# Kernel optimization log

Measured on AMD Instinct MI355X. Metric: run time of the kernel, lower is better.

The kernel has to match this reference:

```python
import jax, jax.numpy as jnp
import numpy as np

VOCAB = 128
N_LAYERS = 4
HEAD_DIM = 128
N_HEADS = 16
PAD = 127
HIDDEN = N_HEADS * HEAD_DIM
B, S = 1, 2048
SCALE = 1.0 / float(np.sqrt(HEAD_DIM))


def _intervals(boundary):
    # torch: interval = cumsum(boundary)+1; shifted = roll(1); shifted[:,0]=interval[:,0]
    idx = jnp.cumsum(boundary.astype(jnp.int32), axis=-1) + 1
    sh = jnp.roll(idx, 1, axis=-1)
    return sh.at[:, 0].set(idx[:, 0])


def _build_mask(tokens, segment_mask, specials_mask):
    # Combined causal & padding & word & segment mask, cache_size=0, distances=0.
    word_int = _intervals(specials_mask)            # [B,S]
    seg_bound = ~segment_mask                       # [B,S]
    seg_int = _intervals(seg_bound)                 # [B,S]
    q = jnp.arange(S)[:, None]
    kv = jnp.arange(S)[None, :]
    causal = q >= kv                                # [S,S]
    dist_neg = (q - kv) < 0                         # mask_*_distance = 0 term
    nonpad = tokens != PAD                          # [B,S]
    padm = nonpad[:, :, None] & nonpad[:, None, :]  # [B,S,S]
    wordm = specials_mask[:, None, :] | dist_neg[None] | (word_int[:, :, None] == word_int[:, None, :])
    segm = seg_bound[:, None, :] | dist_neg[None] | (seg_int[:, :, None] == seg_int[:, None, :])
    return causal[None] & padm & wordm & segm       # [B,S,S]


def _attention(h, mask):
    # q=k=v=h (no projections in DummyModel); flex_attention default scale 1/sqrt(D)
    x = h.reshape(B, S, N_HEADS, HEAD_DIM)
    scores = jnp.einsum('bqhd,bkhd->bhqk', x, x) * SCALE
    neg = jnp.finfo(scores.dtype).min
    scores = jnp.where(mask[:, None], scores, neg)
    probs = jax.nn.softmax(scores, axis=-1)
    # fully-masked rows (e.g. padding queries) -> zero output, matching flex_attention
    row_valid = jnp.any(mask, axis=-1)              # [B,S]
    probs = jnp.where(row_valid[:, None, :, None], probs, 0.0)
    out = jnp.einsum('bhqk,bkhd->bqhd', probs, x)
    return out.reshape(B, S, HIDDEN)


def setup_inputs() -> dict:
    key = jax.random.key(0)
    k1, k2, k3, k4, k5, k6 = jax.random.split(key, 6)
    tokens = jax.random.randint(k1, (B, S), 0, PAD)          # 0..126, no pad tokens
    segment_mask = jax.random.bernoulli(k2, 0.98, (B, S))
    specials_mask = jax.random.bernoulli(k3, 0.2, (B, S))    # True = word boundary/special
    emb_w = jax.random.normal(k4, (VOCAB, HIDDEN), jnp.float32) * 0.02
    lm_w = jax.random.normal(k5, (VOCAB, HIDDEN), jnp.float32) * 0.02
    lm_b = jnp.zeros((VOCAB,), jnp.float32)
    seg_w = jax.random.normal(k6, (2, HIDDEN), jnp.float32) * 0.02
    seg_b = jnp.zeros((2,), jnp.float32)
    return {"tokens": tokens, "segment_mask": segment_mask, "specials_mask": specials_mask,
            "emb_w": emb_w, "lm_w": lm_w, "lm_b": lm_b, "seg_w": seg_w, "seg_b": seg_b}


def reference(tokens, segment_mask, specials_mask, emb_w, lm_w, lm_b, seg_w, seg_b):
    mask = _build_mask(tokens, segment_mask, specials_mask)
    hidden = emb_w[tokens]                                   # [B,S,HIDDEN]
    for _ in range(N_LAYERS):
        hidden = _attention(hidden, mask)
    logits = hidden @ lm_w.T + lm_b                          # [B,S,VOCAB]
    logits_segment = hidden @ seg_w.T + seg_b                # [B,S,2]
    return logits, logits_segment
```

## Files before the change

kernel.cpp:

```cpp
#include <hip/hip_runtime.h>

#define S 2048
#define HID 2048
#define NH 16
#define DH 128
#define VOC 128
#define LCAP 128
#define K2EXP 0.12752551286084112f
#define RTHR 62.0f
#define NEGS -3.0e38f

typedef __bf16 bf16_t;
typedef __attribute__((ext_vector_type(8))) __bf16 bf16x8;
typedef __attribute__((ext_vector_type(4))) __bf16 bf16x4;
typedef __attribute__((ext_vector_type(4))) float f32x4;
typedef __attribute__((ext_vector_type(16))) float f32x16;

typedef __attribute__((address_space(1))) unsigned int guint;
typedef __attribute__((address_space(3))) unsigned int luint;

#define MFMA16 __builtin_amdgcn_mfma_f32_16x16x32_bf16
#define MFMA32 __builtin_amdgcn_mfma_f32_32x32x16_bf16

__device__ __forceinline__ void gl_lds16(const void* g, void* l) {
  __builtin_amdgcn_global_load_lds((guint*)(unsigned long long)g,
                                   (luint*)(unsigned)(unsigned long long)l,
                                   16, 0, 0);
}

__device__ __forceinline__ unsigned cvtpk(float lo, float hi) {
  unsigned r;
  asm("v_cvt_pk_bf16_f32 %0, %1, %2" : "=v"(r) : "v"(lo), "v"(hi));
  return r;
}
__device__ __forceinline__ void plswap(unsigned& a, unsigned& b) {
  asm volatile("v_permlane32_swap_b32 %0, %1" : "+v"(a), "+v"(b));
}
__device__ __forceinline__ bf16x8 mk8(unsigned d0, unsigned d1, unsigned d2, unsigned d3) {
  union { unsigned u[4]; bf16x8 v; } x;
  x.u[0] = d0; x.u[1] = d1; x.u[2] = d2; x.u[3] = d3;
  return x.v;
}


__global__ __launch_bounds__(256) void maskprep2(const int* __restrict__ tokens,
                                                 const unsigned char* __restrict__ seg,
                                                 const unsigned char* __restrict__ spc,
                                                 int4* __restrict__ mi,
                                                 int* __restrict__ lq,
                                                 unsigned long long* __restrict__ lmask,
                                                 int2* __restrict__ smeta) {
  __shared__ int ssp[257], ssg[257], smw[257], sms[257], sfl[257];
  __shared__ int fpre[2048];
  __shared__ int ns64[64];
  __shared__ unsigned long long lmk[32];
  __shared__ int cdet[2];
  int t = threadIdx.x;
  if (t < 2) cdet[t] = 0;
  if (t < 32) lmk[t] = 0ull;
  __syncthreads();
  {
    int nz = ((t & 3) != 0 && seg[t]) ? 1 : 0;
    int fc = ((t & 3) == 3 && seg[t] == 0x3f) ? 1 : 0;
    if (nz) atomicAdd(&cdet[0], 1);
    if (fc) atomicAdd(&cdet[1], 1);
  }
  __syncthreads();
  int lay = (cdet[1] > 8) ? 2 : ((cdet[0] > 4) ? 1 : 0);
  auto getb = [&](const unsigned char* p, int i) -> int {
    if (lay == 1) return p[i] != 0;
    if (lay == 2) return ((const float*)p)[i] != 0.f;
    return ((const int*)p)[i] != 0;
  };
  int base = t * 8;
  int spv[8], sgv[8], npv[8], fv[8];
  int a = 0, b = 0, mw = 0, ms = 0, fs = 0;
  for (int j = 0; j < 8; j++) {
    int i = base + j;
    spv[j] = getb(spc, i);
    sgv[j] = 1 - getb(seg, i);
    npv[j] = (tokens[i] != 127) ? 1 : 0;
    fv[j] = spv[j] & sgv[j] & npv[j];
    a += spv[j]; b += sgv[j]; fs += fv[j];
    if (i >= 1 && spv[j]) mw = (i + 1 > mw) ? i + 1 : mw;
    if (i >= 1 && sgv[j]) ms = (i + 1 > ms) ? i + 1 : ms;
  }
  ssp[t + 1] = a; ssg[t + 1] = b; smw[t + 1] = mw; sms[t + 1] = ms; sfl[t + 1] = fs;
  if (t == 0) { ssp[0] = 0; ssg[0] = 0; smw[0] = 0; sms[0] = 0; sfl[0] = 0; }
  __syncthreads();
  for (int off = 1; off < 256; off <<= 1) {
    int v0 = 0, v1 = 0, v2 = 0, v3 = 0, v4 = 0;
    if (t + 1 > off) { v0 = ssp[t+1-off]; v1 = ssg[t+1-off]; v2 = smw[t+1-off]; v3 = sms[t+1-off]; v4 = sfl[t+1-off]; }
    __syncthreads();
    ssp[t + 1] += v0; ssg[t + 1] += v1;
    if (v2 > smw[t + 1]) smw[t + 1] = v2;
    if (v3 > sms[t + 1]) sms[t + 1] = v3;
    sfl[t + 1] += v4;
    __syncthreads();
  }
  if ((t & 3) == 0) {
    int ws = smw[t], ss = sms[t];
    ns64[t >> 2] = ws < ss ? ws : ss;
  }
  int esp = ssp[t], esg = ssg[t], ef = sfl[t];
  for (int j = 0; j < 8; j++) {
    int i = base + j;
    int wint = (i == 0) ? (1 + spv[j]) : (1 + esp);
    int sint = (i == 0) ? (1 + sgv[j]) : (1 + esg);
    mi[i] = make_int4(npv[j] | (spv[j] << 1) | (sgv[j] << 2), wint, sint, 0);
    fpre[i] = ef;
    int lqv = (fv[j] && ef < LCAP) ? ef : -1;
    lq[i] = lqv;
    if (lqv >= 0) atomicOr(&lmk[i >> 6], 1ull << (i & 63));
    esp += spv[j]; esg += sgv[j]; ef += fv[j];
  }
  __syncthreads();
  if (t < 32) lmask[t] = lmk[t];
  if (t < 64) {
    int nsTile = ns64[t] >> 5;
    int lc = fpre[nsTile * 32];
    if (lc > LCAP) lc = LCAP;
    smeta[t] = make_int2(nsTile, lc);
  }
}

__global__ __launch_bounds__(256) void bitgen(const int4* __restrict__ mi,
                                              unsigned* __restrict__ cmask) {
  __shared__ int4 km[32];
  int w = blockIdx.x;
  int t = threadIdx.x;
  int q = blockIdx.y * 256 + t;
  if (t < 32) km[t] = mi[w * 32 + t];
  __syncthreads();
  int4 mq = mi[q];
  unsigned word = 0;
  #pragma unroll
  for (int j = 0; j < 32; j++) {
    int kv = w * 32 + j;
    int4 mk = km[j];
    bool v = ((mq.x & mk.x) & 1) &&
             ((mk.x & 2) || (mq.y == mk.y)) &&
             ((mk.x & 4) || (mq.z == mk.z)) &&
             (kv <= q);
    word |= (v ? 1u : 0u) << j;
  }
  cmask[(size_t)w * S + q] = word;
}

__global__ __launch_bounds__(256) void embedT2(const int* __restrict__ tokens,
                                               const float* __restrict__ emb,
                                               const int* __restrict__ lq,
                                               const unsigned long long* __restrict__ lmask,
                                               bf16_t* __restrict__ hb, bf16_t* __restrict__ vtb,
                                               bf16_t* __restrict__ hbL, bf16_t* __restrict__ vtbL) {
  __shared__ bf16_t tile[64 * 136];
  int tid = threadIdx.x;
  int q0 = blockIdx.x * 64, h = blockIdx.y;
  int ql = tid >> 2, d0 = (tid & 3) * 32;
  int tok = tokens[q0 + ql];
  const float4* src = (const float4*)(emb + (size_t)tok * HID + h * DH + d0);
  bf16x8 ob[4];
  #pragma unroll
  for (int i = 0; i < 8; i++) {
    float4 f = src[i];
    ob[i >> 1][(i & 1) * 4 + 0] = (bf16_t)f.x;
    ob[i >> 1][(i & 1) * 4 + 1] = (bf16_t)f.y;
    ob[i >> 1][(i & 1) * 4 + 2] = (bf16_t)f.z;
    ob[i >> 1][(i & 1) * 4 + 3] = (bf16_t)f.w;
  }
  #pragma unroll
  for (int i = 0; i < 4; i++)
    *(bf16x8*)(hb + (size_t)(q0 + ql) * HID + h * DH + d0 + i * 8) = ob[i];
  #pragma unroll
  for (int i = 0; i < 4; i++)
    #pragma unroll
    for (int j = 0; j < 8; j++) tile[ql * 136 + d0 + i * 8 + j] = ob[i][j];
  __syncthreads();
  {
    int tl = tid >> 7, d = tid & 127;
    bf16_t* vt = vtb + ((size_t)(h * 64) + 2 * blockIdx.x + tl) * 4096;
    #pragma unroll
    for (int c = 0; c < 4; c++) {
      bf16x8 v;
      #pragma unroll
      for (int e = 0; e < 8; e++)
        v[e] = tile[(32 * tl + 8 * (c ^ (d & 3)) + e) * 136 + d];
      *(bf16x8*)(vt + d * 32 + c * 8) = v;
    }
  }
  unsigned long long lm = lmask[q0 >> 6];
  while (lm) {
    int r = __builtin_ctzll(lm);
    lm &= lm - 1;
    int li = lq[q0 + r];
    if (li >= 0 && tid < 128) {
      bf16_t vv = tile[r * 136 + tid];
      hbL[(size_t)li * HID + h * DH + tid] = vv;
      vtbL[((size_t)(h * 4) + (li >> 5)) * 4096 + tid * 32 + (((li & 31) >> 3) ^ (tid & 3)) * 8 + (li & 7)] = vv;
    }
  }
}

__global__ __launch_bounds__(64, 2) void attn8(const bf16_t* __restrict__ hb,
                                               const bf16_t* __restrict__ vtb,
                                               const bf16_t* __restrict__ hbL,
                                               const bf16_t* __restrict__ vtbL,
                                               const unsigned* __restrict__ cmask,
                                               const int4* __restrict__ mi,
                                               const int2* __restrict__ smeta,
                                               const int* __restrict__ lq,
                                               const unsigned long long* __restrict__ lmask,
                                               bf16_t* __restrict__ ob,
                                               bf16_t* __restrict__ ovtb,
                                               bf16_t* __restrict__ obL,
                                               bf16_t* __restrict__ ovtbL,
                                               int writeT) {
  __shared__ __align__(16) char lds_raw[32768];

  int h = blockIdx.x, st = blockIdx.y;
  int2 sm = smeta[st];
  int nsT = sm.x, lcount = sm.y;
  int nNear = st + 1 - nsT;
  int nLT = (lcount + 31) >> 5;
  int nIter = nNear + nLT;

  int l = threadIdx.x, l31 = l & 31, hi = l >> 5;
  int q0 = 32 * st, q = q0 + l31;
  int npq = mi[q].x & 1;

  bf16x8 qf[8];
  {
    const bf16_t* hq = hb + (size_t)q * HID + h * DH;
    #pragma unroll
    for (int ks = 0; ks < 8; ks++) qf[ks] = *(const bf16x8*)(hq + ks * 16 + hi * 8);
  }

  f32x16 acc[4];
  #pragma unroll
  for (int i = 0; i < 4; i++)
    #pragma unroll
    for (int r = 0; r < 16; r++) acc[i][r] = 0.f;
  float m = -1e30f, lsum = 0.f;
  int swz = l31 & 7;

  auto STAGE = [&](int i, int b) {
    const bf16_t* Kbase; const bf16_t* Vtile;
    if (i < nNear) {
      int t = nsT + i;
      Kbase = hb + (size_t)(t * 32) * HID + h * DH;
      Vtile = vtb + ((size_t)(h * 64) + t) * 4096;
    } else {
      int j = i - nNear;
      Kbase = hbL + (size_t)(j * 32) * HID + h * DH;
      Vtile = vtbL + ((size_t)(h * 4) + j) * 4096;
    }
    bf16_t* Kb = (bf16_t*)(lds_raw + b * 16384);
    bf16_t* Vb = (bf16_t*)(lds_raw + b * 16384 + 8192);
    #pragma unroll
    for (int i2 = 0; i2 < 8; i2++) {
      int rowK = i2 * 4 + (l >> 4); int chK = (l & 15) ^ (rowK & 7);
      gl_lds16(Kbase + (size_t)rowK * HID + chK * 8, Kb + i2 * 512);
    }
    #pragma unroll
    for (int i2 = 0; i2 < 8; i2++)
      gl_lds16(Vtile + i2 * 512 + l * 8, Vb + i2 * 512);
  };

  auto getmask = [&](int i) -> unsigned {
    if (i < nNear) return cmask[(size_t)(nsT + i) * S + q];
    int rem = lcount - (i - nNear) * 32;
    unsigned w0 = (rem >= 32) ? 0xffffffffu : ((rem <= 0) ? 0u : ((1u << rem) - 1u));
    return npq ? w0 : 0u;
  };

  STAGE(0, 0);
  for (int i = 0; i < nIter; i++) {
    int b = i & 1;
    if (i + 1 < nIter) {
      STAGE(i + 1, b ^ 1);
      asm volatile("s_waitcnt vmcnt(16)" ::: "memory");
    } else {
      asm volatile("s_waitcnt vmcnt(0)" ::: "memory");
    }
    unsigned w0 = getmask(i);

    if (__any(w0 != 0u)) {
      const bf16_t* Kb = (const bf16_t*)(lds_raw + b * 16384);
      const bf16_t* Vb = (const bf16_t*)(lds_raw + b * 16384 + 8192);
      f32x16 sA, sB;
      #pragma unroll
      for (int r = 0; r < 16; r++) { sA[r] = 0.f; sB[r] = 0.f; }
      const bf16_t* kp = Kb + l31 * 128;
      #pragma unroll
      for (int ks = 0; ks < 8; ks += 2) {
        bf16x8 kf0 = *(const bf16x8*)(kp + (((2 * ks + hi) ^ swz) * 8));
        bf16x8 kf1 = *(const bf16x8*)(kp + (((2 * (ks + 1) + hi) ^ swz) * 8));
        sA = MFMA32(kf0, qf[ks], sA, 0, 0, 0);
        sB = MFMA32(kf1, qf[ks + 1], sB, 0, 0, 0);
      }

      float sv[16];
      #pragma unroll
      for (int r = 0; r < 16; r++) {
        int bit = (r & 3) + 8 * (r >> 2) + 4 * hi;
        float sr = sA[r] + sB[r];
        sv[r] = ((w0 >> bit) & 1u) ? sr : NEGS;
      }
      float t0 = fmaxf(fmaxf(sv[0], sv[1]), fmaxf(sv[2], sv[3]));
      float t1 = fmaxf(fmaxf(sv[4], sv[5]), fmaxf(sv[6], sv[7]));
      float t2 = fmaxf(fmaxf(sv[8], sv[9]), fmaxf(sv[10], sv[11]));
      float t3 = fmaxf(fmaxf(sv[12], sv[13]), fmaxf(sv[14], sv[15]));
      float mx = fmaxf(fmaxf(t0, t1), fmaxf(t2, t3));
      mx = fmaxf(mx, __shfl_xor(mx, 32, 64));
      if (__any(mx > m + RTHR)) {
        float mn = fmaxf(m, mx);
        float al = exp2f((m - mn) * K2EXP);
        m = mn; lsum *= al;
        #pragma unroll
        for (int r = 0; r < 16; r++) {
          float alr = __shfl(al, (r & 3) + 8 * (r >> 2) + 4 * hi, 64);
          #pragma unroll
          for (int d = 0; d < 4; d++) acc[d][r] *= alr;
        }
      }
      float mk = m * K2EXP;
      float p[16];
      #pragma unroll
      for (int r = 0; r < 16; r++)
        p[r] = exp2f(__builtin_fmaf(sv[r], K2EXP, -mk));
      float u0 = (p[0] + p[1]) + (p[2] + p[3]);
      float u1 = (p[4] + p[5]) + (p[6] + p[7]);
      float u2 = (p[8] + p[9]) + (p[10] + p[11]);
      float u3 = (p[12] + p[13]) + (p[14] + p[15]);
      float ps = (u0 + u1) + (u2 + u3);
      ps += __shfl_xor(ps, 32, 64);
      lsum += ps;

      bf16x8 pa[2];
      {
        unsigned a0 = cvtpk(p[0], p[1]),   a1 = cvtpk(p[2], p[3]);
        unsigned b0 = cvtpk(p[4], p[5]),   b1 = cvtpk(p[6], p[7]);
        unsigned a2 = cvtpk(p[8], p[9]),   a3 = cvtpk(p[10], p[11]);
        unsigned b2 = cvtpk(p[12], p[13]), b3 = cvtpk(p[14], p[15]);
        plswap(a0, b0); plswap(a1, b1); plswap(a2, b2); plswap(a3, b3);
        pa[0] = mk8(a0, a1, b0, b1);
        pa[1] = mk8(a2, a3, b2, b3);
      }

      #pragma unroll
      for (int db = 0; db < 4; db++) {
        const bf16_t* vr = Vb + (32 * db + l31) * 32;
        #pragma unroll
        for (int ks = 0; ks < 2; ks++) {
          bf16x8 vf = *(const bf16x8*)(vr + (((2 * ks + hi) ^ (l31 & 3)) * 8));
          acc[db] = MFMA32(pa[ks], vf, acc[db], 0, 0, 0);
        }
      }
    }
  }

  bf16_t* tl = (bf16_t*)lds_raw;
  float inv = (lsum > 0.f) ? 1.f / lsum : 0.f;
  #pragma unroll
  for (int r = 0; r < 16; r++) {
    int qr = (r & 3) + 8 * (r >> 2) + 4 * hi;
    float ivr = __shfl(inv, qr, 64);
    #pragma unroll
    for (int db = 0; db < 4; db++)
      tl[qr * 132 + db * 32 + l31] = (bf16_t)(acc[db][r] * ivr);
  }
  {
    int c4 = l & 3;
    #pragma unroll
    for (int g = 0; g < 2; g++) {
      int row = g * 16 + (l >> 2);
      #pragma unroll
      for (int k = 0; k < 4; k++) {
        bf16x8 v = *(const bf16x8*)(tl + row * 132 + c4 * 32 + k * 8);
        *(bf16x8*)(ob + (size_t)(q0 + row) * HID + h * DH + c4 * 32 + k * 8) = v;
      }
    }
  }
  if (writeT) {
    bf16_t* vt = ovtb + ((size_t)(h * 64) + st) * 4096;
    #pragma unroll
    for (int s = 0; s < 8; s++) {
      int d = s * 16 + (l >> 2);
      bf16x8 v;
      #pragma unroll
      for (int e = 0; e < 8; e++)
        v[e] = tl[(8 * ((l & 3) ^ (d & 3)) + e) * 132 + d];
      *(bf16x8*)(vt + s * 512 + l * 8) = v;
    }
    unsigned lm32 = (unsigned)(lmask[st >> 1] >> ((st & 1) * 32));
    while (lm32) {
      int r = __builtin_ctz(lm32);
      lm32 &= lm32 - 1;
      int li = lq[q0 + r];
      if (li >= 0) {
        #pragma unroll
        for (int half = 0; half < 2; half++) {
          int dd = l + 64 * half;
          bf16_t vv = tl[r * 132 + dd];
          obL[(size_t)li * HID + h * DH + dd] = vv;
          ovtbL[((size_t)(h * 4) + (li >> 5)) * 4096 + dd * 32 + (((li & 31) >> 3) ^ (dd & 3)) * 8 + (li & 7)] = vv;
        }
      }
    }
  }
}

__global__ __launch_bounds__(256) void wcvt(const float* __restrict__ w, bf16_t* __restrict__ wb) {
  int i = blockIdx.x * 256 + threadIdx.x;
  float4 f = ((const float4*)w)[i];
  bf16x4 v;
  v[0] = (bf16_t)f.x; v[1] = (bf16_t)f.y; v[2] = (bf16_t)f.z; v[3] = (bf16_t)f.w;
  *(bf16x4*)(wb + (size_t)i * 4) = v;
}

__global__ __launch_bounds__(256) void lmseg_head(const bf16_t* __restrict__ hb,
                                                  const bf16_t* __restrict__ wbf,
                                                  const float* __restrict__ bias,
                                                  const float* __restrict__ sw,
                                                  const float* __restrict__ sb,
                                                  float* __restrict__ out,
                                                  float* __restrict__ outseg) {
  __shared__ float red[4][16][130];
  int tid = threadIdx.x;
  int w = tid >> 6, l = tid & 63, l16 = l & 15, g = l >> 4;
  int t0 = blockIdx.x * 16;
  f32x4 acc[8];
  #pragma unroll
  for (int i = 0; i < 8; i++) acc[i] = (f32x4){0.f, 0.f, 0.f, 0.f};
  const bf16_t* arow = hb + (size_t)(t0 + l16) * HID + w * 512;
  for (int k0 = 0; k0 < 512; k0 += 32) {
    bf16x8 af = *(const bf16x8*)(arow + k0 + g * 8);
    #pragma unroll
    for (int vt = 0; vt < 8; vt++) {
      bf16x8 bf_ = *(const bf16x8*)(wbf + (size_t)(vt * 16 + l16) * HID + w * 512 + k0 + g * 8);
      acc[vt] = MFMA16(af, bf_, acc[vt], 0, 0, 0);
    }
  }
  #pragma unroll
  for (int vt = 0; vt < 8; vt++)
    #pragma unroll
    for (int r = 0; r < 4; r++)
      red[w][4 * g + r][vt * 16 + l16] = acc[vt][r];
  __syncthreads();
  int q = tid >> 4, vc = (tid & 15) * 8;
  #pragma unroll
  for (int j = 0; j < 8; j++) {
    float s = red[0][q][vc + j] + red[1][q][vc + j] + red[2][q][vc + j] + red[3][q][vc + j];
    out[(size_t)(t0 + q) * VOC + vc + j] = s + bias[vc + j];
  }
  {
    int c = tid & 15;
    const bf16_t* hrow = hb + (size_t)(t0 + q) * HID + c * 128;
    float s0 = 0.f, s1 = 0.f;
    #pragma unroll
    for (int i = 0; i < 16; i++) {
      bf16x8 v = *(const bf16x8*)(hrow + i * 8);
      const float4* w0p = (const float4*)(sw + c * 128 + i * 8);
      const float4* w1p = (const float4*)(sw + HID + c * 128 + i * 8);
      float4 x0 = w0p[0], x1 = w0p[1], y0 = w1p[0], y1 = w1p[1];
      s0 += (float)v[0]*x0.x + (float)v[1]*x0.y + (float)v[2]*x0.z + (float)v[3]*x0.w
          + (float)v[4]*x1.x + (float)v[5]*x1.y + (float)v[6]*x1.z + (float)v[7]*x1.w;
      s1 += (float)v[0]*y0.x + (float)v[1]*y0.y + (float)v[2]*y0.z + (float)v[3]*y0.w
          + (float)v[4]*y1.x + (float)v[5]*y1.y + (float)v[6]*y1.z + (float)v[7]*y1.w;
    }
    #pragma unroll
    for (int off = 1; off < 16; off <<= 1) {
      s0 += __shfl_xor(s0, off, 64);
      s1 += __shfl_xor(s1, off, 64);
    }
    if (c == 0) {
      outseg[(size_t)(t0 + q) * 2] = s0 + sb[0];
      outseg[(size_t)(t0 + q) * 2 + 1] = s1 + sb[1];
    }
  }
}

extern "C" void kernel_launch(void* const* d_in, const int* in_sizes, int n_in,
                              void* d_out, int out_size, void* d_ws, size_t ws_size,
                              hipStream_t stream) {
  const int* tokens = (const int*)d_in[0];
  const unsigned char* seg = (const unsigned char*)d_in[1];
  const unsigned char* spc = (const unsigned char*)d_in[2];
  const float* emb_w = (const float*)d_in[3];
  const float* lm_w = (const float*)d_in[4];
  const float* lm_b = (const float*)d_in[5];
  const float* seg_w = (const float*)d_in[6];
  const float* seg_b = (const float*)d_in[7];

  char* ws = (char*)d_ws;
  int4* mi = (int4*)ws;
  unsigned* cmask = (unsigned*)(ws + (1u << 20));
  int* lq = (int*)(ws + (1u << 20) + (512u << 10));
  unsigned long long* lmask = (unsigned long long*)(ws + (1u << 20) + (520u << 10));
  int2* smeta = (int2*)(ws + (1u << 20) + (524u << 10));
  bf16_t* wbf = (bf16_t*)(ws + (2u << 20));
  bf16_t* hbLA  = (bf16_t*)(ws + (3u << 20));
  bf16_t* hbLB  = (bf16_t*)(ws + (3u << 20) + (512u << 10));
  bf16_t* vtbLA = (bf16_t*)(ws + (4u << 20));
  bf16_t* vtbLB = (bf16_t*)(ws + (4u << 20) + (512u << 10));
  bf16_t* hbA  = (bf16_t*)(ws + (8u << 20));
  bf16_t* hbB  = (bf16_t*)(ws + (16u << 20));
  bf16_t* vtbA = (bf16_t*)(ws + (24u << 20));
  bf16_t* vtbB = (bf16_t*)(ws + (32u << 20));
  float* out = (float*)d_out;

  maskprep2<<<1, 256, 0, stream>>>(tokens, seg, spc, mi, lq, lmask, smeta);
  bitgen<<<dim3(64, 8), 256, 0, stream>>>(mi, cmask);
  embedT2<<<dim3(S / 64, NH), 256, 0, stream>>>(tokens, emb_w, lq, lmask, hbA, vtbA, hbLA, vtbLA);

  bf16_t* cur = hbA;   bf16_t* curV = vtbA;
  bf16_t* nxt = hbB;   bf16_t* nxtV = vtbB;
  bf16_t* curL = hbLA; bf16_t* curLV = vtbLA;
  bf16_t* nxtL = hbLB; bf16_t* nxtLV = vtbLB;
  for (int L = 0; L < 4; L++) {
    attn8<<<dim3(NH, 64), 64, 0, stream>>>(cur, curV, curL, curLV, cmask, mi, smeta, lq, lmask,
                                           nxt, nxtV, nxtL, nxtLV, (L < 3) ? 1 : 0);
    bf16_t* t1 = cur; cur = nxt; nxt = t1;
    bf16_t* t2 = curV; curV = nxtV; nxtV = t2;
    bf16_t* t3 = curL; curL = nxtL; nxtL = t3;
    bf16_t* t4 = curLV; curLV = nxtLV; nxtLV = t4;
  }

  wcvt<<<(VOC * HID / 4) / 256, 256, 0, stream>>>(lm_w, wbf);
  lmseg_head<<<S / 16, 256, 0, stream>>>(cur, wbf, lm_b, seg_w, seg_b, out, out + (size_t)S * VOC);
}
```

Measured before the change: 137.6 us.

## Store K in pre-swizzled tile layout and merge prep kernels into one launch

The attention kernel now reads K from a contiguous, pre-swizzled per-head 32x128 tile layout (ktb), the same way it reads V, rather than from strided rows of the row-major hidden buffer. Each layer writes its output directly in this tiled K and transposed V form, and writes row-major hidden only on the last layer for the LM head. The bitgen, embedding and weight-convert kernels are merged into a single megaprep launch with block-index dispatch, removing two launches. The cost is an extra tiled write per layer in place of the row-major write, plus more complex indexing.

Result: faster. 121.7 us (-11.5%).

```diff
diff --git a/kernel.cpp b/kernel.cpp
--- a/kernel.cpp
+++ b/kernel.cpp
@@ -124,96 +124,120 @@
   }
 }
 
-__global__ __launch_bounds__(256) void bitgen(const int4* __restrict__ mi,
-                                              unsigned* __restrict__ cmask) {
-  __shared__ int4 km[32];
-  int w = blockIdx.x;
-  int t = threadIdx.x;
-  int q = blockIdx.y * 256 + t;
-  if (t < 32) km[t] = mi[w * 32 + t];
-  __syncthreads();
-  int4 mq = mi[q];
-  unsigned word = 0;
-  #pragma unroll
-  for (int j = 0; j < 32; j++) {
-    int kv = w * 32 + j;
-    int4 mk = km[j];
-    bool v = ((mq.x & mk.x) & 1) &&
-             ((mk.x & 2) || (mq.y == mk.y)) &&
-             ((mk.x & 4) || (mq.z == mk.z)) &&
-             (kv <= q);
-    word |= (v ? 1u : 0u) << j;
-  }
-  cmask[(size_t)w * S + q] = word;
-}
-
-__global__ __launch_bounds__(256) void embedT2(const int* __restrict__ tokens,
-                                               const float* __restrict__ emb,
-                                               const int* __restrict__ lq,
-                                               const unsigned long long* __restrict__ lmask,
-                                               bf16_t* __restrict__ hb, bf16_t* __restrict__ vtb,
-                                               bf16_t* __restrict__ hbL, bf16_t* __restrict__ vtbL) {
-  __shared__ bf16_t tile[64 * 136];
+__global__ __launch_bounds__(256) void megaprep(const int* __restrict__ tokens,
+                                                const float* __restrict__ emb,
+                                                const int4* __restrict__ mi,
+                                                const int* __restrict__ lq,
+                                                const unsigned long long* __restrict__ lmask,
+                                                const float* __restrict__ lm_w,
+                                                bf16_t* __restrict__ wbf,
+                                                unsigned* __restrict__ cmask,
+                                                bf16_t* __restrict__ ktb,
+                                                bf16_t* __restrict__ vtb,
+                                                bf16_t* __restrict__ ktbL,
+                                                bf16_t* __restrict__ vtbL) {
+  __shared__ __align__(16) bf16_t tile[64 * 136];
+  int bid = blockIdx.x;
   int tid = threadIdx.x;
-  int q0 = blockIdx.x * 64, h = blockIdx.y;
-  int ql = tid >> 2, d0 = (tid & 3) * 32;
-  int tok = tokens[q0 + ql];
-  const float4* src = (const float4*)(emb + (size_t)tok * HID + h * DH + d0);
-  bf16x8 ob[4];
-  #pragma unroll
-  for (int i = 0; i < 8; i++) {
-    float4 f = src[i];
-    ob[i >> 1][(i & 1) * 4 + 0] = (bf16_t)f.x;
-    ob[i >> 1][(i & 1) * 4 + 1] = (bf16_t)f.y;
-    ob[i >> 1][(i & 1) * 4 + 2] = (bf16_t)f.z;
-    ob[i >> 1][(i & 1) * 4 + 3] = (bf16_t)f.w;
-  }
-  #pragma unroll
-  for (int i = 0; i < 4; i++)
-    *(bf16x8*)(hb + (size_t)(q0 + ql) * HID + h * DH + d0 + i * 8) = ob[i];
-  #pragma unroll
-  for (int i = 0; i < 4; i++)
-    #pragma unroll
-    for (int j = 0; j < 8; j++) tile[ql * 136 + d0 + i * 8 + j] = ob[i][j];
-  __syncthreads();
-  {
-    int tl = tid >> 7, d = tid & 127;
-    bf16_t* vt = vtb + ((size_t)(h * 64) + 2 * blockIdx.x + tl) * 4096;
-    #pragma unroll
-    for (int c = 0; c < 4; c++) {
-      bf16x8 v;
-      #pragma unroll
-      for (int e = 0; e < 8; e++)
-        v[e] = tile[(32 * tl + 8 * (c ^ (d & 3)) + e) * 136 + d];
-      *(bf16x8*)(vt + d * 32 + c * 8) = v;
-    }
-  }
-  unsigned long long lm = lmask[q0 >> 6];
-  while (lm) {
-    int r = __builtin_ctzll(lm);
-    lm &= lm - 1;
-    int li = lq[q0 + r];
-    if (li >= 0 && tid < 128) {
-      bf16_t vv = tile[r * 136 + tid];
-      hbL[(size_t)li * HID + h * DH + tid] = vv;
-      vtbL[((size_t)(h * 4) + (li >> 5)) * 4096 + tid * 32 + (((li & 31) >> 3) ^ (tid & 3)) * 8 + (li & 7)] = vv;
-    }
-  }
-}
-
-__global__ __launch_bounds__(64, 2) void attn8(const bf16_t* __restrict__ hb,
+
+  if (bid < 512) {
+    int qblk = bid & 31, h = bid >> 5;
+    int q0 = qblk * 64;
+    int ql = tid >> 2, d0 = (tid & 3) * 32;
+    int tok = tokens[q0 + ql];
+    const float4* src = (const float4*)(emb + (size_t)tok * HID + h * DH + d0);
+    #pragma unroll
+    for (int i = 0; i < 8; i++) {
+      float4 f = src[i];
+      tile[ql * 136 + d0 + i * 4 + 0] = (bf16_t)f.x;
+      tile[ql * 136 + d0 + i * 4 + 1] = (bf16_t)f.y;
+      tile[ql * 136 + d0 + i * 4 + 2] = (bf16_t)f.z;
+      tile[ql * 136 + d0 + i * 4 + 3] = (bf16_t)f.w;
+    }
+    __syncthreads();
+    {
+      int tl2 = tid >> 7, half = (tid >> 6) & 1, lane = tid & 63;
+      bf16_t* kt = ktb + ((size_t)(h * 64) + 2 * qblk + tl2) * 4096;
+      #pragma unroll
+      for (int k = 0; k < 4; k++) {
+        int s = half * 4 + k;
+        int row = s * 4 + (lane >> 4);
+        int c = lane & 15;
+        bf16x8 v;
+        #pragma unroll
+        for (int e = 0; e < 8; e++)
+          v[e] = tile[(32 * tl2 + row) * 136 + 8 * (c ^ (row & 7)) + e];
+        *(bf16x8*)(kt + s * 512 + lane * 8) = v;
+      }
+    }
+    {
+      int tl2 = tid >> 7, d = tid & 127;
+      bf16_t* vt = vtb + ((size_t)(h * 64) + 2 * qblk + tl2) * 4096;
+      #pragma unroll
+      for (int c = 0; c < 4; c++) {
+        bf16x8 v;
+        #pragma unroll
+        for (int e = 0; e < 8; e++)
+          v[e] = tile[(32 * tl2 + 8 * (c ^ (d & 3)) + e) * 136 + d];
+        *(bf16x8*)(vt + d * 32 + c * 8) = v;
+      }
+    }
+    unsigned long long lm = lmask[q0 >> 6];
+    while (lm) {
+      int r = __builtin_ctzll(lm);
+      lm &= lm - 1;
+      int li = lq[q0 + r];
+      if (li >= 0 && tid < 128) {
+        int dd = tid;
+        bf16_t vv = tile[r * 136 + dd];
+        int row = li & 31, jt = li >> 5;
+        ktbL[((size_t)(h * 4) + jt) * 4096 + row * 128 + ((dd >> 3) ^ (row & 7)) * 8 + (dd & 7)] = vv;
+        vtbL[((size_t)(h * 4) + jt) * 4096 + dd * 32 + ((row >> 3) ^ (dd & 3)) * 8 + (row & 7)] = vv;
+      }
+    }
+  } else if (bid < 1024) {
+    __shared__ int4 km[32];
+    int b2 = bid - 512;
+    int w = b2 & 63, y = b2 >> 6;
+    int q = y * 256 + tid;
+    if (tid < 32) km[tid] = mi[w * 32 + tid];
+    __syncthreads();
+    int4 mq = mi[q];
+    unsigned word = 0;
+    #pragma unroll
+    for (int j = 0; j < 32; j++) {
+      int kv = w * 32 + j;
+      int4 mk = km[j];
+      bool v = ((mq.x & mk.x) & 1) &&
+               ((mk.x & 2) || (mq.y == mk.y)) &&
+               ((mk.x & 4) || (mq.z == mk.z)) &&
+               (kv <= q);
+      word |= (v ? 1u : 0u) << j;
+    }
+    cmask[(size_t)w * S + q] = word;
+  } else {
+    int i = (bid - 1024) * 256 + tid;
+    float4 f = ((const float4*)lm_w)[i];
+    bf16x4 v;
+    v[0] = (bf16_t)f.x; v[1] = (bf16_t)f.y; v[2] = (bf16_t)f.z; v[3] = (bf16_t)f.w;
+    *(bf16x4*)(wbf + (size_t)i * 4) = v;
+  }
+}
+
+__global__ __launch_bounds__(64, 2) void attn9(const bf16_t* __restrict__ ktb,
                                                const bf16_t* __restrict__ vtb,
-                                               const bf16_t* __restrict__ hbL,
+                                               const bf16_t* __restrict__ ktbL,
                                                const bf16_t* __restrict__ vtbL,
                                                const unsigned* __restrict__ cmask,
                                                const int4* __restrict__ mi,
                                                const int2* __restrict__ smeta,
                                                const int* __restrict__ lq,
                                                const unsigned long long* __restrict__ lmask,
-                                               bf16_t* __restrict__ ob,
+                                               bf16_t* __restrict__ oktb,
                                                bf16_t* __restrict__ ovtb,
-                                               bf16_t* __restrict__ obL,
+                                               bf16_t* __restrict__ oktbL,
                                                bf16_t* __restrict__ ovtbL,
+                                               bf16_t* __restrict__ hbF,
                                                int writeT) {
   __shared__ __align__(16) char lds_raw[32768];
 
@@ -227,12 +251,14 @@
   int l = threadIdx.x, l31 = l & 31, hi = l >> 5;
   int q0 = 32 * st, q = q0 + l31;
   int npq = mi[q].x & 1;
+  int swz = l31 & 7;
 
   bf16x8 qf[8];
   {
-    const bf16_t* hq = hb + (size_t)q * HID + h * DH;
-    #pragma unroll
-    for (int ks = 0; ks < 8; ks++) qf[ks] = *(const bf16x8*)(hq + ks * 16 + hi * 8);
+    const bf16_t* kt0 = ktb + ((size_t)(h * 64) + st) * 4096;
+    #pragma unroll
+    for (int ks = 0; ks < 8; ks++)
+      qf[ks] = *(const bf16x8*)(kt0 + l31 * 128 + (((2 * ks + hi) ^ swz) * 8));
   }
 
   f32x16 acc[4];
@@ -241,26 +267,23 @@
     #pragma unroll
     for (int r = 0; r < 16; r++) acc[i][r] = 0.f;
   float m = -1e30f, lsum = 0.f;
-  int swz = l31 & 7;
 
   auto STAGE = [&](int i, int b) {
-    const bf16_t* Kbase; const bf16_t* Vtile;
+    const bf16_t* Ktile; const bf16_t* Vtile;
     if (i < nNear) {
       int t = nsT + i;
-      Kbase = hb + (size_t)(t * 32) * HID + h * DH;
+      Ktile = ktb + ((size_t)(h * 64) + t) * 4096;
       Vtile = vtb + ((size_t)(h * 64) + t) * 4096;
     } else {
       int j = i - nNear;
-      Kbase = hbL + (size_t)(j * 32) * HID + h * DH;
+      Ktile = ktbL + ((size_t)(h * 4) + j) * 4096;
       Vtile = vtbL + ((size_t)(h * 4) + j) * 4096;
     }
     bf16_t* Kb = (bf16_t*)(lds_raw + b * 16384);
     bf16_t* Vb = (bf16_t*)(lds_raw + b * 16384 + 8192);
     #pragma unroll
-    for (int i2 = 0; i2 < 8; i2++) {
-      int rowK = i2 * 4 + (l >> 4); int chK = (l & 15) ^ (rowK & 7);
-      gl_lds16(Kbase + (size_t)rowK * HID + chK * 8, Kb + i2 * 512);
-    }
+    for (int i2 = 0; i2 < 8; i2++)
+      gl_lds16(Ktile + i2 * 512 + l * 8, Kb + i2 * 512);
     #pragma unroll
     for (int i2 = 0; i2 < 8; i2++)
       gl_lds16(Vtile + i2 * 512 + l * 8, Vb + i2 * 512);
@@ -369,19 +392,18 @@
     for (int db = 0; db < 4; db++)
       tl[qr * 132 + db * 32 + l31] = (bf16_t)(acc[db][r] * ivr);
   }
-  {
-    int c4 = l & 3;
-    #pragma unroll
-    for (int g = 0; g < 2; g++) {
-      int row = g * 16 + (l >> 2);
-      #pragma unroll
-      for (int k = 0; k < 4; k++) {
-        bf16x8 v = *(const bf16x8*)(tl + row * 132 + c4 * 32 + k * 8);
-        *(bf16x8*)(ob + (size_t)(q0 + row) * HID + h * DH + c4 * 32 + k * 8) = v;
-      }
-    }
-  }
   if (writeT) {
+    bf16_t* kt = oktb + ((size_t)(h * 64) + st) * 4096;
+    #pragma unroll
+    for (int s = 0; s < 8; s++) {
+      int row = s * 4 + (l >> 4);
+      int c = l & 15;
+      bf16x8 v;
+      #pragma unroll
+      for (int e = 0; e < 8; e++)
+        v[e] = tl[row * 132 + 8 * (c ^ (row & 7)) + e];
+      *(bf16x8*)(kt + s * 512 + l * 8) = v;
+    }
     bf16_t* vt = ovtb + ((size_t)(h * 64) + st) * 4096;
     #pragma unroll
     for (int s = 0; s < 8; s++) {
@@ -398,24 +420,28 @@
       lm32 &= lm32 - 1;
       int li = lq[q0 + r];
       if (li >= 0) {
+        int row = li & 31, jt = li >> 5;
         #pragma unroll
         for (int half = 0; half < 2; half++) {
           int dd = l + 64 * half;
           bf16_t vv = tl[r * 132 + dd];
-          obL[(size_t)li * HID + h * DH + dd] = vv;
-          ovtbL[((size_t)(h * 4) + (li >> 5)) * 4096 + dd * 32 + (((li & 31) >> 3) ^ (dd & 3)) * 8 + (li & 7)] = vv;
+          oktbL[((size_t)(h * 4) + jt) * 4096 + row * 128 + ((dd >> 3) ^ (row & 7)) * 8 + (dd & 7)] = vv;
+          ovtbL[((size_t)(h * 4) + jt) * 4096 + dd * 32 + ((row >> 3) ^ (dd & 3)) * 8 + (row & 7)] = vv;
         }
       }
     }
-  }
-}
-
-__global__ __launch_bounds__(256) void wcvt(const float* __restrict__ w, bf16_t* __restrict__ wb) {
-  int i = blockIdx.x * 256 + threadIdx.x;
-  float4 f = ((const float4*)w)[i];
-  bf16x4 v;
-  v[0] = (bf16_t)f.x; v[1] = (bf16_t)f.y; v[2] = (bf16_t)f.z; v[3] = (bf16_t)f.w;
-  *(bf16x4*)(wb + (size_t)i * 4) = v;
+  } else {
+    int c4 = l & 3;
+    #pragma unroll
+    for (int g = 0; g < 2; g++) {
+      int row = g * 16 + (l >> 2);
+      #pragma unroll
+      for (int k = 0; k < 4; k++) {
+        bf16x8 v = *(const bf16x8*)(tl + row * 132 + c4 * 32 + k * 8);
+        *(bf16x8*)(hbF + (size_t)(q0 + row) * HID + h * DH + c4 * 32 + k * 8) = v;
+      }
+    }
+  }
 }
 
 __global__ __launch_bounds__(256) void lmseg_head(const bf16_t* __restrict__ hb,
@@ -499,33 +525,33 @@
   unsigned long long* lmask = (unsigned long long*)(ws + (1u << 20) + (520u << 10));
   int2* smeta = (int2*)(ws + (1u << 20) + (524u << 10));
   bf16_t* wbf = (bf16_t*)(ws + (2u << 20));
-  bf16_t* hbLA  = (bf16_t*)(ws + (3u << 20));
-  bf16_t* hbLB  = (bf16_t*)(ws + (3u << 20) + (512u << 10));
+  bf16_t* ktbLA = (bf16_t*)(ws + (3u << 20));
+  bf16_t* ktbLB = (bf16_t*)(ws + (3u << 20) + (512u << 10));
   bf16_t* vtbLA = (bf16_t*)(ws + (4u << 20));
   bf16_t* vtbLB = (bf16_t*)(ws + (4u << 20) + (512u << 10));
-  bf16_t* hbA  = (bf16_t*)(ws + (8u << 20));
-  bf16_t* hbB  = (bf16_t*)(ws + (16u << 20));
-  bf16_t* vtbA = (bf16_t*)(ws + (24u << 20));
-  bf16_t* vtbB = (bf16_t*)(ws + (32u << 20));
+  bf16_t* hbF  = (bf16_t*)(ws + (8u << 20));
+  bf16_t* ktbA = (bf16_t*)(ws + (16u << 20));
+  bf16_t* ktbB = (bf16_t*)(ws + (24u << 20));
+  bf16_t* vtbA = (bf16_t*)(ws + (32u << 20));
+  bf16_t* vtbB = (bf16_t*)(ws + (40u << 20));
   float* out = (float*)d_out;
 
   maskprep2<<<1, 256, 0, stream>>>(tokens, seg, spc, mi, lq, lmask, smeta);
-  bitgen<<<dim3(64, 8), 256, 0, stream>>>(mi, cmask);
-  embedT2<<<dim3(S / 64, NH), 256, 0, stream>>>(tokens, emb_w, lq, lmask, hbA, vtbA, hbLA, vtbLA);
-
-  bf16_t* cur = hbA;   bf16_t* curV = vtbA;
-  bf16_t* nxt = hbB;   bf16_t* nxtV = vtbB;
-  bf16_t* curL = hbLA; bf16_t* curLV = vtbLA;
-  bf16_t* nxtL = hbLB; bf16_t* nxtLV = vtbLB;
+  megaprep<<<1280, 256, 0, stream>>>(tokens, emb_w, mi, lq, lmask, lm_w, wbf, cmask,
+                                     ktbA, vtbA, ktbLA, vtbLA);
+
+  bf16_t* curK = ktbA;  bf16_t* curV = vtbA;
+  bf16_t* nxtK = ktbB;  bf16_t* nxtV = vtbB;
+  bf16_t* curKL = ktbLA; bf16_t* curVL = vtbLA;
+  bf16_t* nxtKL = ktbLB; bf16_t* nxtVL = vtbLB;
   for (int L = 0; L < 4; L++) {
-    attn8<<<dim3(NH, 64), 64, 0, stream>>>(cur, curV, curL, curLV, cmask, mi, smeta, lq, lmask,
-                                           nxt, nxtV, nxtL, nxtLV, (L < 3) ? 1 : 0);
-    bf16_t* t1 = cur; cur = nxt; nxt = t1;
+    attn9<<<dim3(NH, 64), 64, 0, stream>>>(curK, curV, curKL, curVL, cmask, mi, smeta, lq, lmask,
+                                           nxtK, nxtV, nxtKL, nxtVL, hbF, (L < 3) ? 1 : 0);
+    bf16_t* t1 = curK; curK = nxtK; nxtK = t1;
     bf16_t* t2 = curV; curV = nxtV; nxtV = t2;
-    bf16_t* t3 = curL; curL = nxtL; nxtL = t3;
-    bf16_t* t4 = curLV; curLV = nxtLV; nxtLV = t4;
-  }
-
-  wcvt<<<(VOC * HID / 4) / 256, 256, 0, stream>>>(lm_w, wbf);
-  lmseg_head<<<S / 16, 256, 0, stream>>>(cur, wbf, lm_b, seg_w, seg_b, out, out + (size_t)S * VOC);
-}
+    bf16_t* t3 = curKL; curKL = nxtKL; nxtKL = t3;
+    bf16_t* t4 = curVL; curVL = nxtVL; nxtVL = t4;
+  }
+
+  lmseg_head<<<S / 16, 256, 0, stream>>>(hbF, wbf, lm_b, seg_w, seg_b, out, out + (size_t)S * VOC);
+}
```
